# Optimization experiments

Hardware: AMD Instinct MI355X
Metric: run time of the kernel (lower is better)

## Reference

```python
import jax, jax.numpy as jnp
import numpy as np

BETA = 0.25


def setup_inputs() -> dict:
    key = jax.random.key(0)
    k1, k2 = jax.random.split(key)
    z = jax.random.normal(k1, (16, 2048, 256), dtype=jnp.float32)
    # n_q=4 codebooks, each [n_e=2048, e_dim=256]; xavier-ish scale
    W = jax.random.normal(k2, (4, 2048, 256), dtype=jnp.float32) * 0.05
    return {"z": z, "W": W}


def reference(z, W):
    """Residual VQ forward (p=1.0, eval-mode math). Returns (z_q, loss, indices)."""
    n_q, n_e, e_dim = W.shape
    lead = z.shape[:-1]
    flat_shape = (-1, e_dim)

    residual = z
    cumulative_q = jnp.zeros_like(z)
    losses = []
    idx_list = []
    for k in range(n_q):
        Wk = W[k]  # [n_e, e_dim]
        flat = residual.reshape(flat_shape)  # [N, e_dim]
        dist = (
            jnp.sum(flat * flat, axis=1, keepdims=True)
            - 2.0 * (flat @ Wk.T)
            + jnp.sum(Wk * Wk, axis=1)[None, :]
        )
        idx = jnp.argmin(dist, axis=1)  # [N]
        # one_hot @ Wk is mathematically a gather of codebook rows
        q = Wk[idx].reshape(residual.shape)
        # commit + beta*codebook; both are (residual.detach() - q)^2.mean(-1)
        diff = jax.lax.stop_gradient(residual) - q
        losses.append((1.0 + BETA) * jnp.mean(diff * diff, axis=-1))
        cumulative_q = cumulative_q + q
        residual = residual - q
        idx_list.append(idx.reshape(*lead, 1))

    # straight-through: gradient of z_q flows only to z
    z_q = z + jax.lax.stop_gradient(cumulative_q - z)
    total_loss = jnp.mean(jnp.stack(losses, axis=0).mean(axis=0))
    indices = jnp.concatenate(idx_list, axis=-1)  # [..., n_q]
    return z_q, total_loss, indices
```

## Files before the change

### kernel.cpp

```cpp
#include <hip/hip_runtime.h>
#include <cstdint>
#include <math.h>
#include <float.h>

#define N_Q   4
#define NROWS 32768
#define EDIM  256
#define NE    2048
#define NCT_H 64
#define TM    64
#define NTHREADS 256

#define ZQ_SIZE  (NROWS * EDIM)
#define LOSS_OFF ZQ_SIZE
#define IDX_OFF  (ZQ_SIZE + 1)

#define TAU 0.012f

typedef __attribute__((ext_vector_type(8))) _Float16 f16x8;
typedef __attribute__((ext_vector_type(4))) float    f32x4;

union F8 { _Float16 h[8]; f16x8 v; };

__device__ __forceinline__ float np_block128_sq(const float* __restrict__ p) {
    #pragma clang fp contract(off)
    float r[8];
    #pragma unroll
    for (int j = 0; j < 8; ++j) { float v = p[j]; r[j] = v * v; }
    for (int i = 8; i < 128; i += 8) {
        #pragma unroll
        for (int j = 0; j < 8; ++j) { float v = p[i + j]; float sq = v * v; r[j] = r[j] + sq; }
    }
    return ((r[0] + r[1]) + (r[2] + r[3])) + ((r[4] + r[5]) + (r[6] + r[7]));
}

__global__ __launch_bounds__(256) void wsq_kernel(const float* __restrict__ W,
                                                  float* __restrict__ wsq32) {
    __shared__ float rowbuf[4][EDIM];
    int wv   = threadIdx.x >> 6;
    int row  = blockIdx.x * 4 + (threadIdx.x >> 6);
    int lane = threadIdx.x & 63;
    float4 v = ((const float4*)(W + (size_t)row * EDIM))[lane];
    *(float4*)&rowbuf[wv][lane * 4] = v;
    __syncthreads();
    if (lane == 0) {
        float a = np_block128_sq(rowbuf[wv]);
        float b = np_block128_sq(rowbuf[wv] + 128);
        wsq32[row] = a + b;
    }
}

__global__ __launch_bounds__(256) void wh_kernel(const float* __restrict__ W,
                                                 short* __restrict__ wh) {
    int gid  = blockIdx.x * 256 + threadIdx.x;
    int lane = gid & 63;
    int grp  = gid >> 6;
    int ctq  = grp >> 3;
    int ks   = grp & 7;
    int n = lane & 15, kq = lane >> 4;
    const float* src = W + (((size_t)(ctq * 16 + n)) << 8) + ks * 32 + kq * 8;
    float4 p0 = *(const float4*)src;
    float4 p1 = *(const float4*)(src + 4);
    float v[8] = {p0.x, p0.y, p0.z, p0.w, p1.x, p1.y, p1.z, p1.w};
    F8 h;
    #pragma unroll
    for (int j = 0; j < 8; ++j) h.h[j] = (_Float16)v[j];
    *(f16x8*)(wh + (((size_t)grp) << 9) + lane * 8) = h.v;
}

__device__ __forceinline__ void top3_merge(float& a1, int& ai1, float& a2, int& ai2, float& a3,
                                           float b1, int bi1, float b2, int bi2, float b3) {
    float c1, c2, c3; int k1, k2;
    if (b1 < a1 || (b1 == a1 && bi1 < ai1)) {
        c1 = b1; k1 = bi1;
        if (a1 < b2 || (a1 == b2 && ai1 < bi2)) { c2 = a1; k2 = ai1; c3 = fminf(b2, a2); }
        else                                    { c2 = b2; k2 = bi2; c3 = fminf(a1, b3); }
    } else {
        c1 = a1; k1 = ai1;
        if (b1 < a2 || (b1 == a2 && bi1 < ai2)) { c2 = b1; k2 = bi1; c3 = fminf(a2, b2); }
        else                                    { c2 = a2; k2 = ai2; c3 = fminf(b1, a3); }
    }
    a1 = c1; ai1 = k1; a2 = c2; ai2 = k2; a3 = c3;
}

__global__ __launch_bounds__(256, 2) void rvq_main(
    const float* __restrict__ z, const float* __restrict__ W,
    const float* __restrict__ wsq32, const short* __restrict__ wh,
    float* __restrict__ resd_g, float* __restrict__ out,
    float* __restrict__ loss_partial)
{
    __shared__ __align__(16) short lds_b[2][2][4][512];
    __shared__ float Srow[TM];
    __shared__ float rm1[2][TM], rm2[2][TM], rm3[2][TM];
    __shared__ int   ri1[2][TM], ri2[2][TM];
    __shared__ int   idx_s[TM], is2_s[TM];
    __shared__ int   rk_cnt, rk_list[TM];
    __shared__ int   pr_cnt, pr_list[TM];
    __shared__ float rrow_s[EDIM];
    __shared__ float red_f[NTHREADS];
    __shared__ int   red_i[NTHREADS];
    __shared__ float wavesum[4];

    const int tid  = threadIdx.x;
    const int wave = tid >> 6;
    const int lane = tid & 63;
    const int n    = lane & 15;
    const int kq   = lane >> 4;
    const int half = wave >> 1;
    const int rsel = wave & 1;
    const int row0 = blockIdx.x * TM;
    const int rowg = row0 + rsel * 32;

    for (int i = tid; i < TM * 64; i += NTHREADS) {
        int r = i >> 6, c = i & 63;
        ((float4*)resd_g)[(((size_t)(row0 + r)) << 6) + c] =
            ((const float4*)z)[(((size_t)(row0 + r)) << 6) + c];
    }

    float lsum = 0.f;

    for (int q = 0; q < N_Q; ++q) {
        const float* Wk   = W + (size_t)q * NE * EDIM;
        const float* wsqk = wsq32 + q * NE;
        const short* whq  = wh + ((size_t)q << 19);

        __syncthreads();
        if (tid == 0) { rk_cnt = 0; pr_cnt = 0; }
        if (tid < 2 * TM) {
            int r = tid >> 1, hf = tid & 1;
            float s = np_block128_sq(resd_g + (((size_t)(row0 + r)) << 8) + hf * 128);
            float s2 = __shfl_xor(s, 1, 64);
            if (hf == 0) Srow[r] = s + s2;
        }
        __syncthreads();

        f16x8 ah[2][8];
        #pragma unroll
        for (int t = 0; t < 2; ++t) {
            #pragma unroll
            for (int ks = 0; ks < 8; ++ks) {
                const float* rp = resd_g + (((size_t)(rowg + t * 16 + n)) << 8) + ks * 32 + kq * 8;
                float4 p0 = *(const float4*)rp;
                float4 p1 = *(const float4*)(rp + 4);
                float v[8] = {p0.x, p0.y, p0.z, p0.w, p1.x, p1.y, p1.z, p1.w};
                F8 h;
                #pragma unroll
                for (int j = 0; j < 8; ++j) h.h[j] = (_Float16)v[j];
                ah[t][ks] = h.v;
            }
        }
        float sreg[2][4];
        #pragma unroll
        for (int t = 0; t < 2; ++t)
            #pragma unroll
            for (int rg = 0; rg < 4; ++rg)
                sreg[t][rg] = Srow[rsel * 32 + t * 16 + kq * 4 + rg];

        float M1[8], M2[8], M3[8]; int I1[8], I2[8];
        #pragma unroll
        for (int s = 0; s < 8; ++s) {
            M1[s] = INFINITY; M2[s] = INFINITY; M3[s] = INFINITY; I1[s] = 0; I2[s] = 0;
        }

        auto stage = [&](int buf, int ct, int kp) {
            #pragma unroll
            for (int j = 0; j < 2; ++j) {
                int ksl = (wave & 1) * 2 + j;
                size_t grp = ((size_t)((wave >> 1) * 64 + ct) << 3) + kp * 4 + ksl;
                const short* gp = whq + (grp << 9) + lane * 8;
                __builtin_amdgcn_global_load_lds(
                    (const __attribute__((address_space(1))) void*)gp,
                    (__attribute__((address_space(3))) void*)&lds_b[buf][wave >> 1][ksl][0],
                    16, 0, 0);
            }
        };

        f32x4 acc[2];
        stage(0, 0, 0);
        __syncthreads();

        for (int ct = 0; ct < NCT_H; ++ct) {
            float wq = wsqk[(half * 64 + ct) * 16 + n];

            stage(1, ct, 1);
            acc[0] = (f32x4){0.f, 0.f, 0.f, 0.f};
            acc[1] = (f32x4){0.f, 0.f, 0.f, 0.f};
            #pragma unroll
            for (int ksl = 0; ksl < 4; ++ksl) {
                f16x8 bh = *(const f16x8*)&lds_b[0][half][ksl][lane * 8];
                acc[0] = __builtin_amdgcn_mfma_f32_16x16x32_f16(ah[0][ksl], bh, acc[0], 0, 0, 0);
                acc[1] = __builtin_amdgcn_mfma_f32_16x16x32_f16(ah[1][ksl], bh, acc[1], 0, 0, 0);
            }
            __syncthreads();

            if (ct + 1 < NCT_H) stage(0, ct + 1, 0);
            #pragma unroll
            for (int ksl = 0; ksl < 4; ++ksl) {
                f16x8 bh = *(const f16x8*)&lds_b[1][half][ksl][lane * 8];
                const int ks = 4 + ksl;
                acc[0] = __builtin_amdgcn_mfma_f32_16x16x32_f16(ah[0][ks], bh, acc[0], 0, 0, 0);
                acc[1] = __builtin_amdgcn_mfma_f32_16x16x32_f16(ah[1][ks], bh, acc[1], 0, 0, 0);
            }

            int cg = (half * 64 + ct) * 16 + n;
            #pragma unroll
            for (int t = 0; t < 2; ++t) {
                #pragma unroll
                for (int rg = 0; rg < 4; ++rg) {
                    float d = fmaf(-2.0f, acc[t][rg], sreg[t][rg]) + wq;
                    int s = t * 4 + rg;
                    bool c1 = d < M1[s];
                    bool c2 = d < M2[s];
                    M3[s] = fminf(M3[s], fmaxf(M2[s], d));
                    M2[s] = fminf(M2[s], fmaxf(M1[s], d));
                    I2[s] = c1 ? I1[s] : (c2 ? cg : I2[s]);
                    M1[s] = fminf(M1[s], d);
                    I1[s] = c1 ? cg : I1[s];
                }
            }
            __syncthreads();
        }

        #pragma unroll
        for (int s = 0; s < 8; ++s) {
            float a1 = M1[s], a2 = M2[s], a3 = M3[s]; int ai = I1[s], aj = I2[s];
            #pragma unroll
            for (int mask = 1; mask < 16; mask <<= 1) {
                float b1 = __shfl_xor(a1, mask, 64);
                float b2 = __shfl_xor(a2, mask, 64);
                float b3 = __shfl_xor(a3, mask, 64);
                int   bi = __shfl_xor(ai, mask, 64);
                int   bj = __shfl_xor(aj, mask, 64);
                top3_merge(a1, ai, a2, aj, a3, b1, bi, b2, bj, b3);
            }
            if (n == 0) {
                int rr = rsel * 32 + (s >> 2) * 16 + kq * 4 + (s & 3);
                rm1[half][rr] = a1; rm2[half][rr] = a2; rm3[half][rr] = a3;
                ri1[half][rr] = ai; ri2[half][rr] = aj;
            }
        }
        __syncthreads();

        if (tid < TM) {
            float a1 = rm1[0][tid], a2 = rm2[0][tid], a3 = rm3[0][tid];
            int ai = ri1[0][tid], aj = ri2[0][tid];
            top3_merge(a1, ai, a2, aj, a3,
                       rm1[1][tid], ri1[1][tid], rm2[1][tid], ri2[1][tid], rm3[1][tid]);
            idx_s[tid] = ai; is2_s[tid] = aj;
            if (a2 - a1 <= TAU) {
                if (a3 - a1 > TAU) { int p = atomicAdd(&pr_cnt, 1); pr_list[p] = tid; }
                else               { int p = atomicAdd(&rk_cnt, 1); rk_list[p] = tid; }
            }
        }
        __syncthreads();

        {
            int ncheck = rk_cnt;
            for (int f = 0; f < ncheck; ++f) {
                int r = rk_list[f];
                if (tid < 64)
                    ((float4*)rrow_s)[tid] =
                        ((const float4*)(resd_g + (((size_t)(row0 + r)) << 8)))[tid];
                __syncthreads();
                float Sr = Srow[r];
                float accv[8];
                #pragma unroll
                for (int j = 0; j < 8; ++j) accv[j] = 0.f;
                const float* wp = Wk + ((size_t)tid * 8) * EDIM;
                for (int kb = 0; kb < 64; ++kb) {
                    float4 rv = *(const float4*)&rrow_s[kb * 4];
                    #pragma unroll
                    for (int j = 0; j < 8; ++j) {
                        float4 wv = *(const float4*)(wp + j * EDIM + kb * 4);
                        accv[j] = fmaf(rv.x, wv.x, accv[j]);
                        accv[j] = fmaf(rv.y, wv.y, accv[j]);
                        accv[j] = fmaf(rv.z, wv.z, accv[j]);
                        accv[j] = fmaf(rv.w, wv.w, accv[j]);
                    }
                }
                float bm = FLT_MAX; int bi = 0;
                #pragma unroll
                for (int j = 0; j < 8; ++j) {
                    int c = tid * 8 + j;
                    float d = fmaf(-2.0f, accv[j], Sr) + wsqk[c];
                    if (d < bm) { bm = d; bi = c; }
                }
                red_f[tid] = bm; red_i[tid] = bi;
                __syncthreads();
                for (int off = 128; off > 0; off >>= 1) {
                    if (tid < off) {
                        float v = red_f[tid + off]; int ii = red_i[tid + off];
                        if (v < red_f[tid] || (v == red_f[tid] && ii < red_i[tid])) {
                            red_f[tid] = v; red_i[tid] = ii;
                        }
                    }
                    __syncthreads();
                }
                if (tid == 0) idx_s[r] = red_i[0];
                __syncthreads();
            }
        }

        {
            int cnt2 = pr_cnt * 2;
            for (int base = 0; base < cnt2; base += NTHREADS) {
                int slot = base + tid;
                float d = FLT_MAX; int code = 0; int r = -1;
                if (slot < cnt2) {
                    r = pr_list[slot >> 1];
                    code = (slot & 1) ? is2_s[r] : idx_s[r];
                    const float* rp = resd_g + (((size_t)(row0 + r)) << 8);
                    const float* wp = Wk + ((size_t)code << 8);
                    float acc1 = 0.f;
                    for (int kb = 0; kb < 64; ++kb) {
                        float4 rv = *(const float4*)(rp + kb * 4);
                        float4 wv = *(const float4*)(wp + kb * 4);
                        acc1 = fmaf(rv.x, wv.x, acc1);
                        acc1 = fmaf(rv.y, wv.y, acc1);
                        acc1 = fmaf(rv.z, wv.z, acc1);
                        acc1 = fmaf(rv.w, wv.w, acc1);
                    }
                    d = fmaf(-2.0f, acc1, Srow[r]) + wsqk[code];
                }
                float dp = __shfl_xor(d, 1, 64);
                int   cp = __shfl_xor(code, 1, 64);
                if (slot < cnt2 && (slot & 1) == 0) {
                    idx_s[r] = (dp < d || (dp == d && cp < code)) ? cp : code;
                }
            }
        }
        __syncthreads();

        if (tid < TM)
            out[IDX_OFF + (size_t)(row0 + tid) * N_Q + q] = (float)idx_s[tid];
        __syncthreads();

        {
            const int d = tid;
            for (int r = 0; r < TM; ++r) {
                float w = Wk[(((size_t)idx_s[r]) << 8) + d];
                float* rp = resd_g + (((size_t)(row0 + r)) << 8) + d;
                float nv = *rp - w;
                *rp = nv;
                lsum = fmaf(nv, nv, lsum);
            }
        }
    }

    __syncthreads();
    for (int i = tid; i < TM * 64; i += NTHREADS) {
        int r = i >> 6, c = i & 63;
        float4 zv = ((const float4*)z)[(((size_t)(row0 + r)) << 6) + c];
        float4 rv = ((const float4*)resd_g)[(((size_t)(row0 + r)) << 6) + c];
        float4 o = {zv.x - rv.x, zv.y - rv.y, zv.z - rv.z, zv.w - rv.w};
        ((float4*)out)[(((size_t)(row0 + r)) << 6) + c] = o;
    }
    #pragma unroll
    for (int off = 32; off > 0; off >>= 1) lsum += __shfl_down(lsum, off, 64);
    if (lane == 0) wavesum[wave] = lsum;
    __syncthreads();
    if (tid == 0)
        loss_partial[blockIdx.x] = wavesum[0] + wavesum[1] + wavesum[2] + wavesum[3];
}

__global__ __launch_bounds__(256) void loss_reduce(const float* __restrict__ partial,
                                                   float* __restrict__ out) {
    __shared__ float sh[256];
    int t = threadIdx.x;
    sh[t] = partial[t] + partial[t + 256];
    __syncthreads();
    for (int off = 128; off > 0; off >>= 1) {
        if (t < off) sh[t] += sh[t + off];
        __syncthreads();
    }
    if (t == 0)
        out[LOSS_OFF] = sh[0] * (1.25f / ((float)N_Q * (float)NROWS * (float)EDIM));
}

extern "C" void kernel_launch(void* const* d_in, const int* in_sizes, int n_in,
                              void* d_out, int out_size, void* d_ws, size_t ws_size,
                              hipStream_t stream) {
    const float* z = (const float*)d_in[0];
    const float* W = (const float*)d_in[1];
    float* out = (float*)d_out;

    float* wsq32   = (float*)d_ws;
    float* partial = (float*)((char*)d_ws + 32768);
    short* wh      = (short*)((char*)d_ws + 65536);
    float* resd    = (float*)((char*)d_ws + 65536 + 8388608);

    hipLaunchKernelGGL(wsq_kernel, dim3(NE * N_Q / 4), dim3(NTHREADS), 0, stream, W, wsq32);
    hipLaunchKernelGGL(wh_kernel, dim3(1024), dim3(NTHREADS), 0, stream, W, wh);
    hipLaunchKernelGGL(rvq_main, dim3(NROWS / TM), dim3(NTHREADS), 0, stream,
                       z, W, wsq32, wh, resd, out, partial);
    hipLaunchKernelGGL(loss_reduce, dim3(1), dim3(NTHREADS), 0, stream, partial, out);
}
```

Baseline: 622.2 us.

## Give each wave private 4-deep codebook LDS buffers and drop per-tile block barriers

The codebook-tile loop is restructured so each wave streams its own fp16 codebook tiles into a private 4-slot LDS ring. Waits use explicit vmcnt counts, so the two __syncthreads per column tile go away. Codeword norms are preloaded into LDS, and the per-row norm term is dropped from the distance because it is constant per row and does not change the argmin or top-3 gaps. Scratch arrays are aliased onto the ring to keep LDS use down. In exchange, waves that share a column half now fetch the same tiles twice, doubling L2 traffic for B, and LDS per block grows.

```diff
diff --git a/kernel.cpp b/kernel.cpp
--- a/kernel.cpp
+++ b/kernel.cpp
@@ -7,7 +7,7 @@
 #define NROWS 32768
 #define EDIM  256
 #define NE    2048
-#define NCT_H 64
+#define NCT   64
 #define TM    64
 #define NTHREADS 256
 
@@ -89,25 +89,27 @@
     float* __restrict__ resd_g, float* __restrict__ out,
     float* __restrict__ loss_partial)
 {
-    __shared__ __align__(16) short lds_b[2][2][4][512];
+    __shared__ __align__(16) short lds_b[4][4][4][512];
+    __shared__ float wsq_lds[2048];
     __shared__ float Srow[TM];
     __shared__ float rm1[2][TM], rm2[2][TM], rm3[2][TM];
     __shared__ int   ri1[2][TM], ri2[2][TM];
     __shared__ int   idx_s[TM], is2_s[TM];
     __shared__ int   rk_cnt, rk_list[TM];
     __shared__ int   pr_cnt, pr_list[TM];
-    __shared__ float rrow_s[EDIM];
-    __shared__ float red_f[NTHREADS];
-    __shared__ int   red_i[NTHREADS];
     __shared__ float wavesum[4];
+
+    float* rrow_s = (float*)&lds_b[0][0][0][0];
+    float* red_f  = (float*)&lds_b[1][0][0][0];
+    int*   red_i  = (int*)  &lds_b[1][1][0][0];
 
     const int tid  = threadIdx.x;
     const int wave = tid >> 6;
     const int lane = tid & 63;
     const int n    = lane & 15;
     const int kq   = lane >> 4;
-    const int half = wave >> 1;
-    const int rsel = wave & 1;
+    const int chalf = wave & 1;
+    const int rsel  = wave >> 1;
     const int row0 = blockIdx.x * TM;
     const int rowg = row0 + rsel * 32;
 
@@ -132,7 +134,8 @@
             float s2 = __shfl_xor(s, 1, 64);
             if (hf == 0) Srow[r] = s + s2;
         }
-        __syncthreads();
+        for (int i = tid; i < 512; i += NTHREADS)
+            ((float4*)wsq_lds)[i] = ((const float4*)wsqk)[i];
 
         f16x8 ah[2][8];
         #pragma unroll
@@ -149,12 +152,7 @@
                 ah[t][ks] = h.v;
             }
         }
-        float sreg[2][4];
-        #pragma unroll
-        for (int t = 0; t < 2; ++t)
-            #pragma unroll
-            for (int rg = 0; rg < 4; ++rg)
-                sreg[t][rg] = Srow[rsel * 32 + t * 16 + kq * 4 + rg];
+        __syncthreads();
 
         float M1[8], M2[8], M3[8]; int I1[8], I2[8];
         #pragma unroll
@@ -162,52 +160,66 @@
             M1[s] = INFINITY; M2[s] = INFINITY; M3[s] = INFINITY; I1[s] = 0; I2[s] = 0;
         }
 
-        auto stage = [&](int buf, int ct, int kp) {
+        auto stage = [&](int p) {
+            int ct = p >> 1, kp = p & 1;
+            int b = p & 3;
             #pragma unroll
-            for (int j = 0; j < 2; ++j) {
-                int ksl = (wave & 1) * 2 + j;
-                size_t grp = ((size_t)((wave >> 1) * 64 + ct) << 3) + kp * 4 + ksl;
+            for (int ksl = 0; ksl < 4; ++ksl) {
+                size_t grp = ((size_t)(chalf * 64 + ct) << 3) + kp * 4 + ksl;
                 const short* gp = whq + (grp << 9) + lane * 8;
                 __builtin_amdgcn_global_load_lds(
                     (const __attribute__((address_space(1))) void*)gp,
-                    (__attribute__((address_space(3))) void*)&lds_b[buf][wave >> 1][ksl][0],
+                    (__attribute__((address_space(3))) void*)&lds_b[wave][b][ksl][0],
                     16, 0, 0);
             }
         };
 
+        asm volatile("s_waitcnt vmcnt(0)" ::: "memory");
+        stage(0);
+        stage(1);
+
         f32x4 acc[2];
-        stage(0, 0, 0);
-        __syncthreads();
-
-        for (int ct = 0; ct < NCT_H; ++ct) {
-            float wq = wsqk[(half * 64 + ct) * 16 + n];
-
-            stage(1, ct, 1);
-            acc[0] = (f32x4){0.f, 0.f, 0.f, 0.f};
-            acc[1] = (f32x4){0.f, 0.f, 0.f, 0.f};
-            #pragma unroll
-            for (int ksl = 0; ksl < 4; ++ksl) {
-                f16x8 bh = *(const f16x8*)&lds_b[0][half][ksl][lane * 8];
-                acc[0] = __builtin_amdgcn_mfma_f32_16x16x32_f16(ah[0][ksl], bh, acc[0], 0, 0, 0);
-                acc[1] = __builtin_amdgcn_mfma_f32_16x16x32_f16(ah[1][ksl], bh, acc[1], 0, 0, 0);
-            }
-            __syncthreads();
-
-            if (ct + 1 < NCT_H) stage(0, ct + 1, 0);
-            #pragma unroll
-            for (int ksl = 0; ksl < 4; ++ksl) {
-                f16x8 bh = *(const f16x8*)&lds_b[1][half][ksl][lane * 8];
-                const int ks = 4 + ksl;
-                acc[0] = __builtin_amdgcn_mfma_f32_16x16x32_f16(ah[0][ks], bh, acc[0], 0, 0, 0);
-                acc[1] = __builtin_amdgcn_mfma_f32_16x16x32_f16(ah[1][ks], bh, acc[1], 0, 0, 0);
-            }
-
-            int cg = (half * 64 + ct) * 16 + n;
+        for (int ct = 0; ct < NCT; ++ct) {
+            float wq = wsq_lds[chalf * 1024 + ct * 16 + n];
+
+            asm volatile("s_waitcnt vmcnt(4)" ::: "memory");
+            __builtin_amdgcn_sched_barrier(0);
+            {
+                const int b = (2 * ct) & 3;
+                acc[0] = (f32x4){0.f, 0.f, 0.f, 0.f};
+                acc[1] = (f32x4){0.f, 0.f, 0.f, 0.f};
+                #pragma unroll
+                for (int ksl = 0; ksl < 4; ++ksl) {
+                    f16x8 bh = *(const f16x8*)&lds_b[wave][b][ksl][lane * 8];
+                    acc[0] = __builtin_amdgcn_mfma_f32_16x16x32_f16(ah[0][ksl], bh, acc[0], 0, 0, 0);
+                    acc[1] = __builtin_amdgcn_mfma_f32_16x16x32_f16(ah[1][ksl], bh, acc[1], 0, 0, 0);
+                }
+            }
+            if (ct < NCT - 1) stage(2 * ct + 2);
+
+            if (ct < NCT - 1) {
+                asm volatile("s_waitcnt vmcnt(4)" ::: "memory");
+            } else {
+                asm volatile("s_waitcnt vmcnt(0)" ::: "memory");
+            }
+            __builtin_amdgcn_sched_barrier(0);
+            {
+                const int b = (2 * ct + 1) & 3;
+                #pragma unroll
+                for (int ksl = 0; ksl < 4; ++ksl) {
+                    f16x8 bh = *(const f16x8*)&lds_b[wave][b][ksl][lane * 8];
+                    acc[0] = __builtin_amdgcn_mfma_f32_16x16x32_f16(ah[0][4 + ksl], bh, acc[0], 0, 0, 0);
+                    acc[1] = __builtin_amdgcn_mfma_f32_16x16x32_f16(ah[1][4 + ksl], bh, acc[1], 0, 0, 0);
+                }
+            }
+            if (ct < NCT - 1) stage(2 * ct + 3);
+
+            int cg = chalf * 1024 + ct * 16 + n;
             #pragma unroll
             for (int t = 0; t < 2; ++t) {
                 #pragma unroll
                 for (int rg = 0; rg < 4; ++rg) {
-                    float d = fmaf(-2.0f, acc[t][rg], sreg[t][rg]) + wq;
+                    float d = fmaf(-2.0f, acc[t][rg], wq);
                     int s = t * 4 + rg;
                     bool c1 = d < M1[s];
                     bool c2 = d < M2[s];
@@ -218,7 +230,6 @@
                     I1[s] = c1 ? cg : I1[s];
                 }
             }
-            __syncthreads();
         }
 
         #pragma unroll
@@ -235,8 +246,8 @@
             }
             if (n == 0) {
                 int rr = rsel * 32 + (s >> 2) * 16 + kq * 4 + (s & 3);
-                rm1[half][rr] = a1; rm2[half][rr] = a2; rm3[half][rr] = a3;
-                ri1[half][rr] = ai; ri2[half][rr] = aj;
+                rm1[chalf][rr] = a1; rm2[chalf][rr] = a2; rm3[chalf][rr] = a3;
+                ri1[chalf][rr] = ai; ri2[chalf][rr] = aj;
             }
         }
         __syncthreads();
```

Result: faster. 592.0 us (-4.8%).
